# Optimization experiments

Hardware: AMD Instinct MI355X
Metric: run time of the kernel (lower is better)

## Reference

```python
import jax, jax.numpy as jnp
import numpy as np

EMBED_DIM = 768
HEADS = 8
HEAD_DIM = 128  # gnn_hidden_dim
OUT_DIM = HEADS * HEAD_DIM  # 1024, concat=True
NEG_SLOPE = 0.2  # PyG GATConv leaky_relu slope


def setup_inputs() -> dict:
    key = jax.random.key(0)
    ks = jax.random.split(key, 12)
    N, E = 10000, 160000
    x = jax.random.normal(ks[0], (N, EMBED_DIM), dtype=jnp.float32)
    edge_index = jax.random.randint(ks[1], (2, E), 0, N, dtype=jnp.int32)
    edge_attr = jax.random.uniform(ks[2], (E, 1), dtype=jnp.float32)
    # GATConv params (single layer, edge_dim=1)
    sc = 1.0 / np.sqrt(EMBED_DIM)
    W = jax.random.normal(ks[3], (EMBED_DIM, OUT_DIM), dtype=jnp.float32) * sc
    att_src = jax.random.normal(ks[4], (HEADS, HEAD_DIM), dtype=jnp.float32) * 0.1
    att_dst = jax.random.normal(ks[5], (HEADS, HEAD_DIM), dtype=jnp.float32) * 0.1
    W_edge = jax.random.normal(ks[6], (1, OUT_DIM), dtype=jnp.float32)
    att_edge = jax.random.normal(ks[7], (HEADS, HEAD_DIM), dtype=jnp.float32) * 0.1
    bias = jnp.zeros((OUT_DIM,), dtype=jnp.float32)
    # final classifier: in = 3*OUT_DIM (global pool + text node + image node)
    clf_W = jax.random.normal(ks[8], (3 * OUT_DIM, 2), dtype=jnp.float32) * (1.0 / np.sqrt(3 * OUT_DIM))
    clf_b = jnp.zeros((2,), dtype=jnp.float32)
    return {
        'x': x, 'edge_index': edge_index, 'edge_attr': edge_attr,
        'text_idx': 0, 'image_idx': 1,
        'W': W, 'att_src': att_src, 'att_dst': att_dst,
        'W_edge': W_edge, 'att_edge': att_edge, 'bias': bias,
        'clf_W': clf_W, 'clf_b': clf_b,
    }


def gat_layer(x, edge_index, edge_attr, W, att_src, att_dst, W_edge, att_edge, bias):
    N = x.shape[0]
    # add self-loops with edge_attr = mean of existing edge_attr (PyG default fill_value='mean')
    loop = jnp.arange(N, dtype=edge_index.dtype)
    ei = jnp.concatenate([edge_index, jnp.stack([loop, loop])], axis=1)
    ea_mean = jnp.mean(edge_attr, axis=0, keepdims=True)
    ea = jnp.concatenate([edge_attr, jnp.broadcast_to(ea_mean, (N, edge_attr.shape[1]))], axis=0)
    src, dst = ei[0], ei[1]
    xs = (x @ W).reshape(N, HEADS, HEAD_DIM)             # [N, H, C]
    a_src = jnp.einsum('nhc,hc->nh', xs, att_src)        # per-node src logits
    a_dst = jnp.einsum('nhc,hc->nh', xs, att_dst)
    e_emb = (ea @ W_edge).reshape(-1, HEADS, HEAD_DIM)   # [Etot, H, C]
    a_edge = jnp.einsum('ehc,hc->eh', e_emb, att_edge)
    alpha = jax.nn.leaky_relu(a_src[src] + a_dst[dst] + a_edge, NEG_SLOPE)  # [Etot, H]
    # softmax over incoming edges of each dst node
    m = jax.ops.segment_max(alpha, dst, num_segments=N)
    ex = jnp.exp(alpha - m[dst])
    denom = jax.ops.segment_sum(ex, dst, num_segments=N)
    w = ex / denom[dst]                                  # normalized attention [Etot, H]
    msg = xs[src] * w[:, :, None]                        # [Etot, H, C]
    out = jax.ops.segment_sum(msg, dst, num_segments=N)  # [N, H, C]
    return out.reshape(N, OUT_DIM) + bias


def reference(x, edge_index, edge_attr, text_idx, image_idx,
              W, att_src, att_dst, W_edge, att_edge, bias, clf_W, clf_b):
    # single GAT layer (num_gat_layers=1 -> no ELU/dropout after, eval mode)
    h = gat_layer(x, edge_index, edge_attr, W, att_src, att_dst, W_edge, att_edge, bias)
    g = jnp.mean(h, axis=0, keepdims=True)               # global_mean_pool, batch=None
    t = h[text_idx][None, :]
    im = h[image_idx][None, :]
    fused = jnp.concatenate([g, t, im], axis=1)          # [1, 3*OUT_DIM]
    logits = fused @ clf_W + clf_b                       # [1, 2]
    return logits
```

## Files before the change

### kernel.cpp

```cpp
#include <hip/hip_runtime.h>

#define NN 10000
#define EE 160000
#define ETOT (EE + NN)
#define EMB 768
#define ODIM 1024
#define NEG 0.2f
#define CAP 56

#define OFF_P      0
#define OFF_Q      12288
#define OFF_EAP    12296
#define OFF_EAACC  12360
#define OFF_CNTD   12364
#define ZERO_START 12364
#define ZERO_CNT   10000
#define OFF_A      22364
#define OFF_T      182364
#define OFF_SAED   342364
#define OFF_RDEN   1462364
#define OFF_G      1542364

#define SELF_MARK 3.0e38f

__global__ __launch_bounds__(256) void k1a(
    const float* __restrict__ W, const float* __restrict__ att_src,
    const float* __restrict__ att_dst, const float* __restrict__ W_edge,
    const float* __restrict__ att_edge, const float* __restrict__ bias,
    const float* __restrict__ clf_W, const float* __restrict__ clf_b,
    float* __restrict__ out, float* __restrict__ ws) {
  __shared__ float sred[8];
  int b = blockIdx.x;
  if (b < 48) {
    int tid = b * 256 + threadIdx.x;
    int k = tid >> 4, j = tid & 15, h = j & 7;
    const float* att = (j < 8) ? att_src : att_dst;
    const float4* wp = (const float4*)(W + k * ODIM + h * 128);
    const float4* ap = (const float4*)(att + h * 128);
    float acc = 0.f;
    #pragma unroll 8
    for (int c = 0; c < 32; ++c) {
      float4 w4 = wp[c], a4 = ap[c];
      acc += w4.x * a4.x + w4.y * a4.y + w4.z * a4.z + w4.w * a4.w;
    }
    ws[OFF_P + tid] = acc;
  } else if (b == 48) {
    if (threadIdx.x < 8) {
      int h = threadIdx.x;
      float acc = 0.f;
      #pragma unroll 8
      for (int c = 0; c < 128; ++c) acc += W_edge[h * 128 + c] * att_edge[h * 128 + c];
      ws[OFF_Q + h] = acc;
    }
  } else if (b == 49) {
    int t = threadIdx.x;
    float b0 = 0.f, b1 = 0.f;
    for (int i = t; i < 3072; i += 256) {
      float f = bias[i & 1023];
      b0 += f * clf_W[2 * i];
      b1 += f * clf_W[2 * i + 1];
    }
    #pragma unroll
    for (int o = 32; o > 0; o >>= 1) {
      b0 += __shfl_down(b0, o, 64);
      b1 += __shfl_down(b1, o, 64);
    }
    if ((t & 63) == 0) { sred[(t >> 6) * 2] = b0; sred[(t >> 6) * 2 + 1] = b1; }
    __syncthreads();
    if (t == 0) {
      out[0] = clf_b[0] + sred[0] + sred[2] + sred[4] + sred[6];
      out[1] = clf_b[1] + sred[1] + sred[3] + sred[5] + sred[7];
    }
  } else {
    int t = (b - 50) * 256 + threadIdx.x;
    int k = t >> 3, h = t & 7;
    const float4* wseg = (const float4*)(W + k * ODIM + h * 128);
    float acc[6] = {0.f, 0.f, 0.f, 0.f, 0.f, 0.f};
    for (int c4 = 0; c4 < 32; ++c4) {
      float4 wv = wseg[c4];
      #pragma unroll
      for (int d = 0; d < 3; ++d) {
        const float4* cp = (const float4*)(clf_W + 2 * (1024 * d + h * 128 + c4 * 4));
        float4 q0 = cp[0], q1 = cp[1];
        acc[d * 2 + 0] += wv.x * q0.x + wv.y * q0.z + wv.z * q1.x + wv.w * q1.z;
        acc[d * 2 + 1] += wv.x * q0.y + wv.y * q0.w + wv.z * q1.y + wv.w * q1.w;
      }
    }
    #pragma unroll
    for (int d = 0; d < 3; ++d) {
      ws[OFF_G + d * 12288 + k * 16 + h * 2 + 0] = acc[d * 2 + 0];
      ws[OFF_G + d * 12288 + k * 16 + h * 2 + 1] = acc[d * 2 + 1];
    }
  }
}

__global__ __launch_bounds__(256) void k1b(const float* __restrict__ edge_attr,
                                           const int* __restrict__ ei,
                                           float* __restrict__ ws) {
  __shared__ float sred[8];
  int b = blockIdx.x;
  if (b < 64) {
    float acc = 0.f;
    for (int i = b * 256 + threadIdx.x; i < EE; i += 64 * 256) acc += edge_attr[i];
    #pragma unroll
    for (int off = 32; off > 0; off >>= 1) acc += __shfl_down(acc, off, 64);
    if ((threadIdx.x & 63) == 0) sred[threadIdx.x >> 6] = acc;
    __syncthreads();
    if (threadIdx.x == 0)
      ws[OFF_EAP + b] = sred[0] + sred[1] + sred[2] + sred[3];
  } else {
    int e = (b - 64) * 256 + threadIdx.x;
    if (e >= ETOT) return;
    int src, dst; float ea;
    if (e < EE) { src = ei[e]; dst = ei[EE + e]; ea = edge_attr[e]; }
    else { src = dst = e - EE; ea = SELF_MARK; }
    int* cntd = (int*)(ws + OFF_CNTD);
    int pd = atomicAdd(&cntd[dst], 1);
    if (pd < CAP) {
      float2 pr; pr.x = __int_as_float(src); pr.y = ea;
      ((float2*)(ws + OFF_SAED))[dst * CAP + pd] = pr;
    }
  }
}

__global__ __launch_bounds__(256) void kAxT(const float* __restrict__ x,
                                            float* __restrict__ ws) {
  __shared__ float smem[12288];
  if (blockIdx.x == 313) {
    if (threadIdx.x < 64) {
      float v = ws[OFF_EAP + threadIdx.x];
      #pragma unroll
      for (int o = 32; o > 0; o >>= 1) v += __shfl_down(v, o, 64);
      if (threadIdx.x == 0) ws[OFF_EAACC] = v;
    }
    return;
  }
  int nl = threadIdx.x & 31, cg = threadIdx.x >> 5;
  int n = blockIdx.x * 32 + nl;
  #pragma unroll
  for (int pass = 0; pass < 2; ++pass) {
    const int tbl = (pass == 0) ? OFF_P : OFF_G;
    const int dstoff = (pass == 0) ? OFF_A : OFF_T;
    for (int i = threadIdx.x; i < 3072; i += 256)
      ((float4*)smem)[i] = ((const float4*)(ws + tbl))[i];
    __syncthreads();
    float a[16];
    #pragma unroll
    for (int j = 0; j < 16; ++j) a[j] = 0.f;
    if (n < NN) {
      const float4* xr = (const float4*)(x + n * EMB + cg * 96);
      for (int kk = 0; kk < 24; ++kk) {
        float4 xv = xr[kk];
        const float* pr = &smem[(cg * 96 + kk * 4) * 16];
        #pragma unroll
        for (int j = 0; j < 16; ++j) a[j] += xv.x * pr[j];
        #pragma unroll
        for (int j = 0; j < 16; ++j) a[j] += xv.y * pr[16 + j];
        #pragma unroll
        for (int j = 0; j < 16; ++j) a[j] += xv.z * pr[32 + j];
        #pragma unroll
        for (int j = 0; j < 16; ++j) a[j] += xv.w * pr[48 + j];
      }
    }
    __syncthreads();
    #pragma unroll
    for (int j = 0; j < 16; ++j) smem[(cg * 16 + j) * 33 + nl] = a[j];
    __syncthreads();
    for (int w = threadIdx.x; w < 512; w += 256) {
      int rnl = w >> 4, j = w & 15;
      int nn = blockIdx.x * 32 + rnl;
      if (nn < NN) {
        float s = 0.f;
        #pragma unroll
        for (int c2 = 0; c2 < 8; ++c2) s += smem[(c2 * 16 + j) * 33 + rnl];
        ws[dstoff + nn * 16 + j] = s;
      }
    }
    __syncthreads();
  }
}

__global__ __launch_bounds__(128) void kD(float* __restrict__ ws) {
  int t = blockIdx.x * 128 + threadIdx.x;
  int dst = t >> 3, h = t & 7;
  int deg = ((const int*)(ws + OFF_CNTD))[dst];
  if (deg > CAP) deg = CAP;
  float adh = ws[OFF_A + dst * 16 + 8 + h];
  float qh = ws[OFF_Q + h];
  float mean = ws[OFF_EAACC] * (1.0f / EE);
  const float2* prow = (const float2*)(ws + OFF_SAED) + dst * CAP;
  float den = 0.f;
  #pragma unroll 4
  for (int j = 0; j < deg; ++j) {
    float2 pr = prow[j];
    int srcj = __float_as_int(pr.x);
    float ae = pr.y;
    if (ae > 1e37f) ae = mean;
    float v = ws[OFF_A + srcj * 16 + h] + adh + ae * qh;
    v = (v >= 0.f) ? v : NEG * v;
    den += __expf(v);
  }
  ws[OFF_RDEN + t] = 1.0f / den;
}

__global__ __launch_bounds__(256, 3) void kFin(const float* __restrict__ x,
                                               const int* __restrict__ ei,
                                               const float* __restrict__ edge_attr,
                                               const int* __restrict__ tptr,
                                               const int* __restrict__ iptr,
                                               float* __restrict__ out,
                                               float* __restrict__ ws) {
  __shared__ float smem[12864];
  int t = threadIdx.x;
  float mean = ws[OFF_EAACC] * (1.0f / EE);
  float c0 = 0.f, c1 = 0.f;
  float scale;
  if (blockIdx.x < 665) {
    scale = 1.0f / NN;
    int e = blockIdx.x * 256 + t;
    if (e < ETOT) {
      int src, dst; float ea;
      if (e < EE) { src = ei[e]; dst = ei[EE + e]; ea = edge_attr[e]; }
      else { src = dst = e - EE; ea = mean; }
      const float4* as4 = (const float4*)(ws + OFF_A + src * 16);
      const float4* ad4 = (const float4*)(ws + OFF_A + dst * 16 + 8);
      const float4* rd4 = (const float4*)(ws + OFF_RDEN + dst * 8);
      const float4* t4  = (const float4*)(ws + OFF_T + src * 16);
      float4 s0 = as4[0], s1 = as4[1], d0 = ad4[0], d1 = ad4[1];
      float4 r0 = rd4[0], r1 = rd4[1];
      float4 t0 = t4[0], t1 = t4[1], t2 = t4[2], t3 = t4[3];
      float asr[8] = {s0.x, s0.y, s0.z, s0.w, s1.x, s1.y, s1.z, s1.w};
      float ads[8] = {d0.x, d0.y, d0.z, d0.w, d1.x, d1.y, d1.z, d1.w};
      float rdn[8] = {r0.x, r0.y, r0.z, r0.w, r1.x, r1.y, r1.z, r1.w};
      float tt[16] = {t0.x, t0.y, t0.z, t0.w, t1.x, t1.y, t1.z, t1.w,
                      t2.x, t2.y, t2.z, t2.w, t3.x, t3.y, t3.z, t3.w};
      #pragma unroll
      for (int h = 0; h < 8; ++h) {
        float v = asr[h] + ads[h] + ea * ws[OFF_Q + h];
        v = (v >= 0.f) ? v : NEG * v;
        float w = __expf(v) * rdn[h];
        c0 += w * tt[2 * h];
        c1 += w * tt[2 * h + 1];
      }
    }
  } else {
    scale = 1.0f;
    int d = blockIdx.x - 665;
    int target = (d == 0) ? tptr[0] : iptr[0];
    for (int i = t; i < 3072; i += 256)
      ((float4*)smem)[i] = ((const float4*)(ws + OFF_G + (d + 1) * 12288))[i];
    int deg = ((const int*)(ws + OFF_CNTD))[target];
    if (deg > CAP) deg = CAP;
    for (int idx = t; idx < deg * 8; idx += 256) {
      int j = idx >> 3, h = idx & 7;
      float2 pr = ((const float2*)(ws + OFF_SAED))[target * CAP + j];
      int srcj = __float_as_int(pr.x);
      float ae = pr.y;
      if (ae > 1e37f) ae = mean;
      float v = ws[OFF_A + srcj * 16 + h] + ws[OFF_A + target * 16 + 8 + h]
              + ae * ws[OFF_Q + h];
      v = (v >= 0.f) ? v : NEG * v;
      smem[12288 + j * 8 + h] = __expf(v) * ws[OFF_RDEN + target * 8 + h];
      if (h == 0) ((int*)smem)[12800 + j] = srcj;
    }
    __syncthreads();
    int nl = t & 15, cgp = t >> 4;
    for (int jb = 0; jb * 16 < deg; ++jb) {
      int j = jb * 16 + nl;
      int n = (j < deg) ? ((int*)smem)[12800 + j] : 0;
      float a[16];
      #pragma unroll
      for (int jj = 0; jj < 16; ++jj) a[jj] = 0.f;
      const float4* xr = (const float4*)(x + n * EMB + cgp * 48);
      for (int kk = 0; kk < 12; ++kk) {
        float4 xv = xr[kk];
        const float* pr = &smem[(cgp * 48 + kk * 4) * 16];
        #pragma unroll
        for (int jj = 0; jj < 16; ++jj) a[jj] += xv.x * pr[jj];
        #pragma unroll
        for (int jj = 0; jj < 16; ++jj) a[jj] += xv.y * pr[16 + jj];
        #pragma unroll
        for (int jj = 0; jj < 16; ++jj) a[jj] += xv.z * pr[32 + jj];
        #pragma unroll
        for (int jj = 0; jj < 16; ++jj) a[jj] += xv.w * pr[48 + jj];
      }
      if (j < deg) {
        #pragma unroll
        for (int h = 0; h < 8; ++h) {
          float wv = smem[12288 + j * 8 + h];
          c0 += wv * a[2 * h];
          c1 += wv * a[2 * h + 1];
        }
      }
    }
  }
  #pragma unroll
  for (int o = 32; o > 0; o >>= 1) {
    c0 += __shfl_down(c0, o, 64);
    c1 += __shfl_down(c1, o, 64);
  }
  if ((t & 63) == 0) {
    smem[12856 + (t >> 6) * 2] = c0;
    smem[12857 + (t >> 6) * 2] = c1;
  }
  __syncthreads();
  if (t == 0) {
    float r0 = smem[12856] + smem[12858] + smem[12860] + smem[12862];
    float r1 = smem[12857] + smem[12859] + smem[12861] + smem[12863];
    atomicAdd(&out[0], r0 * scale);
    atomicAdd(&out[1], r1 * scale);
  }
}

extern "C" void kernel_launch(void* const* d_in, const int* in_sizes, int n_in,
                              void* d_out, int out_size, void* d_ws, size_t ws_size,
                              hipStream_t stream) {
  const float* x        = (const float*)d_in[0];
  const int*   ei       = (const int*)d_in[1];
  const float* edge_attr= (const float*)d_in[2];
  const int*   tptr     = (const int*)d_in[3];
  const int*   iptr     = (const int*)d_in[4];
  const float* W        = (const float*)d_in[5];
  const float* att_src  = (const float*)d_in[6];
  const float* att_dst  = (const float*)d_in[7];
  const float* W_edge   = (const float*)d_in[8];
  const float* att_edge = (const float*)d_in[9];
  const float* bias     = (const float*)d_in[10];
  const float* clf_W    = (const float*)d_in[11];
  const float* clf_b    = (const float*)d_in[12];
  float* ws  = (float*)d_ws;
  float* out = (float*)d_out;

  hipMemsetAsync(ws + ZERO_START, 0, ZERO_CNT * sizeof(float), stream);
  k1a<<<74, 256, 0, stream>>>(W, att_src, att_dst, W_edge, att_edge,
                              bias, clf_W, clf_b, out, ws);
  k1b<<<729, 256, 0, stream>>>(edge_attr, ei, ws);
  kAxT<<<314, 256, 0, stream>>>(x, ws);
  kD<<<625, 128, 0, stream>>>(ws);
  kFin<<<667, 256, 0, stream>>>(x, ei, edge_attr, tptr, iptr, out, ws);
}
```

Before: 193.2 us.

## Fuse pipeline into three kernels and merge softmax denominator into dst-side aggregation

Replaces the memset and five kernels with three launches. Zeroing of the degree counters moves into k1, and CSR bucketing now runs in the same launch as the x·P/x·G projection (k2). The separate denominator kernel and the per-edge final pass become one per-(dst,head) loop that accumulates the exp sum and the weighted T numerator together, so the reciprocal-denominator buffer and its reread go away. This cuts launch gaps and memory traffic. It risks a race: bucketing in k2 reads counters zeroed in k1, which is fine across launches, but k2's projection and bucketing blocks now share one grid, and the per-dst loop has an uneven per-thread degree load.

```diff
diff --git a/kernel.cpp b/kernel.cpp
--- a/kernel.cpp
+++ b/kernel.cpp
@@ -13,22 +13,20 @@
 #define OFF_EAP    12296
 #define OFF_EAACC  12360
 #define OFF_CNTD   12364
-#define ZERO_START 12364
-#define ZERO_CNT   10000
 #define OFF_A      22364
 #define OFF_T      182364
 #define OFF_SAED   342364
-#define OFF_RDEN   1462364
-#define OFF_G      1542364
+#define OFF_G      1462364
 
 #define SELF_MARK 3.0e38f
 
-__global__ __launch_bounds__(256) void k1a(
+__global__ __launch_bounds__(256) void k1(
     const float* __restrict__ W, const float* __restrict__ att_src,
     const float* __restrict__ att_dst, const float* __restrict__ W_edge,
-    const float* __restrict__ att_edge, const float* __restrict__ bias,
-    const float* __restrict__ clf_W, const float* __restrict__ clf_b,
-    float* __restrict__ out, float* __restrict__ ws) {
+    const float* __restrict__ att_edge, const float* __restrict__ edge_attr,
+    const float* __restrict__ bias, const float* __restrict__ clf_W,
+    const float* __restrict__ clf_b, float* __restrict__ out,
+    float* __restrict__ ws) {
   __shared__ float sred[8];
   int b = blockIdx.x;
   if (b < 48) {
@@ -71,7 +69,7 @@
       out[0] = clf_b[0] + sred[0] + sred[2] + sred[4] + sred[6];
       out[1] = clf_b[1] + sred[1] + sred[3] + sred[5] + sred[7];
     }
-  } else {
+  } else if (b < 74) {
     int t = (b - 50) * 256 + threadIdx.x;
     int k = t >> 3, h = t & 7;
     const float4* wseg = (const float4*)(W + k * ODIM + h * 128);
@@ -91,25 +89,38 @@
       ws[OFF_G + d * 12288 + k * 16 + h * 2 + 0] = acc[d * 2 + 0];
       ws[OFF_G + d * 12288 + k * 16 + h * 2 + 1] = acc[d * 2 + 1];
     }
-  }
-}
-
-__global__ __launch_bounds__(256) void k1b(const float* __restrict__ edge_attr,
-                                           const int* __restrict__ ei,
-                                           float* __restrict__ ws) {
-  __shared__ float sred[8];
-  int b = blockIdx.x;
-  if (b < 64) {
+  } else if (b < 138) {
+    int bi = b - 74;
     float acc = 0.f;
-    for (int i = b * 256 + threadIdx.x; i < EE; i += 64 * 256) acc += edge_attr[i];
+    for (int i = bi * 256 + threadIdx.x; i < EE; i += 64 * 256) acc += edge_attr[i];
     #pragma unroll
     for (int off = 32; off > 0; off >>= 1) acc += __shfl_down(acc, off, 64);
     if ((threadIdx.x & 63) == 0) sred[threadIdx.x >> 6] = acc;
     __syncthreads();
     if (threadIdx.x == 0)
-      ws[OFF_EAP + b] = sred[0] + sred[1] + sred[2] + sred[3];
+      ws[OFF_EAP + bi] = sred[0] + sred[1] + sred[2] + sred[3];
   } else {
-    int e = (b - 64) * 256 + threadIdx.x;
+    int i = (b - 138) * 256 + threadIdx.x;
+    if (i < NN) ((int*)(ws + OFF_CNTD))[i] = 0;
+  }
+}
+
+__global__ __launch_bounds__(256) void k2(const float* __restrict__ x,
+                                          const int* __restrict__ ei,
+                                          const float* __restrict__ edge_attr,
+                                          float* __restrict__ ws) {
+  __shared__ float smem[12288];
+  if (blockIdx.x == 313) {
+    if (threadIdx.x < 64) {
+      float v = ws[OFF_EAP + threadIdx.x];
+      #pragma unroll
+      for (int o = 32; o > 0; o >>= 1) v += __shfl_down(v, o, 64);
+      if (threadIdx.x == 0) ws[OFF_EAACC] = v;
+    }
+    return;
+  }
+  if (blockIdx.x >= 314) {
+    int e = (blockIdx.x - 314) * 256 + threadIdx.x;
     if (e >= ETOT) return;
     int src, dst; float ea;
     if (e < EE) { src = ei[e]; dst = ei[EE + e]; ea = edge_attr[e]; }
@@ -120,19 +131,6 @@
       float2 pr; pr.x = __int_as_float(src); pr.y = ea;
       ((float2*)(ws + OFF_SAED))[dst * CAP + pd] = pr;
     }
-  }
-}
-
-__global__ __launch_bounds__(256) void kAxT(const float* __restrict__ x,
-                                            float* __restrict__ ws) {
-  __shared__ float smem[12288];
-  if (blockIdx.x == 313) {
-    if (threadIdx.x < 64) {
-      float v = ws[OFF_EAP + threadIdx.x];
-      #pragma unroll
-      for (int o = 32; o > 0; o >>= 1) v += __shfl_down(v, o, 64);
-      if (threadIdx.x == 0) ws[OFF_EAACC] = v;
-    }
     return;
   }
   int nl = threadIdx.x & 31, cg = threadIdx.x >> 5;
@@ -180,72 +178,48 @@
   }
 }
 
-__global__ __launch_bounds__(128) void kD(float* __restrict__ ws) {
-  int t = blockIdx.x * 128 + threadIdx.x;
-  int dst = t >> 3, h = t & 7;
-  int deg = ((const int*)(ws + OFF_CNTD))[dst];
-  if (deg > CAP) deg = CAP;
-  float adh = ws[OFF_A + dst * 16 + 8 + h];
-  float qh = ws[OFF_Q + h];
-  float mean = ws[OFF_EAACC] * (1.0f / EE);
-  const float2* prow = (const float2*)(ws + OFF_SAED) + dst * CAP;
-  float den = 0.f;
-  #pragma unroll 4
-  for (int j = 0; j < deg; ++j) {
-    float2 pr = prow[j];
-    int srcj = __float_as_int(pr.x);
-    float ae = pr.y;
-    if (ae > 1e37f) ae = mean;
-    float v = ws[OFF_A + srcj * 16 + h] + adh + ae * qh;
-    v = (v >= 0.f) ? v : NEG * v;
-    den += __expf(v);
-  }
-  ws[OFF_RDEN + t] = 1.0f / den;
-}
-
-__global__ __launch_bounds__(256, 3) void kFin(const float* __restrict__ x,
-                                               const int* __restrict__ ei,
-                                               const float* __restrict__ edge_attr,
-                                               const int* __restrict__ tptr,
-                                               const int* __restrict__ iptr,
-                                               float* __restrict__ out,
-                                               float* __restrict__ ws) {
-  __shared__ float smem[12864];
+__global__ __launch_bounds__(256, 3) void k3(const float* __restrict__ x,
+                                             const int* __restrict__ tptr,
+                                             const int* __restrict__ iptr,
+                                             float* __restrict__ out,
+                                             float* __restrict__ ws) {
+  __shared__ float smem[12880];
   int t = threadIdx.x;
   float mean = ws[OFF_EAACC] * (1.0f / EE);
   float c0 = 0.f, c1 = 0.f;
   float scale;
-  if (blockIdx.x < 665) {
+  if (blockIdx.x < 313) {
     scale = 1.0f / NN;
-    int e = blockIdx.x * 256 + t;
-    if (e < ETOT) {
-      int src, dst; float ea;
-      if (e < EE) { src = ei[e]; dst = ei[EE + e]; ea = edge_attr[e]; }
-      else { src = dst = e - EE; ea = mean; }
-      const float4* as4 = (const float4*)(ws + OFF_A + src * 16);
-      const float4* ad4 = (const float4*)(ws + OFF_A + dst * 16 + 8);
-      const float4* rd4 = (const float4*)(ws + OFF_RDEN + dst * 8);
-      const float4* t4  = (const float4*)(ws + OFF_T + src * 16);
-      float4 s0 = as4[0], s1 = as4[1], d0 = ad4[0], d1 = ad4[1];
-      float4 r0 = rd4[0], r1 = rd4[1];
-      float4 t0 = t4[0], t1 = t4[1], t2 = t4[2], t3 = t4[3];
-      float asr[8] = {s0.x, s0.y, s0.z, s0.w, s1.x, s1.y, s1.z, s1.w};
-      float ads[8] = {d0.x, d0.y, d0.z, d0.w, d1.x, d1.y, d1.z, d1.w};
-      float rdn[8] = {r0.x, r0.y, r0.z, r0.w, r1.x, r1.y, r1.z, r1.w};
-      float tt[16] = {t0.x, t0.y, t0.z, t0.w, t1.x, t1.y, t1.z, t1.w,
-                      t2.x, t2.y, t2.z, t2.w, t3.x, t3.y, t3.z, t3.w};
-      #pragma unroll
-      for (int h = 0; h < 8; ++h) {
-        float v = asr[h] + ads[h] + ea * ws[OFF_Q + h];
+    int tk = blockIdx.x * 256 + t;
+    if (tk < 80000) {
+      int dst = tk >> 3, h = tk & 7;
+      int deg = ((const int*)(ws + OFF_CNTD))[dst];
+      if (deg > CAP) deg = CAP;
+      float adh = ws[OFF_A + dst * 16 + 8 + h];
+      float qh = ws[OFF_Q + h];
+      const float2* prow = (const float2*)(ws + OFF_SAED) + dst * CAP;
+      float den = 0.f, n0 = 0.f, n1 = 0.f;
+      #pragma unroll 4
+      for (int j = 0; j < deg; ++j) {
+        float2 pr = prow[j];
+        int srcj = __float_as_int(pr.x);
+        float ae = pr.y;
+        if (ae > 1e37f) ae = mean;
+        float v = ws[OFF_A + srcj * 16 + h] + adh + ae * qh;
         v = (v >= 0.f) ? v : NEG * v;
-        float w = __expf(v) * rdn[h];
-        c0 += w * tt[2 * h];
-        c1 += w * tt[2 * h + 1];
-      }
+        float ex = __expf(v);
+        den += ex;
+        float2 tv = *(const float2*)(ws + OFF_T + srcj * 16 + 2 * h);
+        n0 += ex * tv.x;
+        n1 += ex * tv.y;
+      }
+      float r = 1.0f / den;
+      c0 = n0 * r;
+      c1 = n1 * r;
     }
   } else {
     scale = 1.0f;
-    int d = blockIdx.x - 665;
+    int d = blockIdx.x - 313;
     int target = (d == 0) ? tptr[0] : iptr[0];
     for (int i = t; i < 3072; i += 256)
       ((float4*)smem)[i] = ((const float4*)(ws + OFF_G + (d + 1) * 12288))[i];
@@ -260,8 +234,14 @@
       float v = ws[OFF_A + srcj * 16 + h] + ws[OFF_A + target * 16 + 8 + h]
               + ae * ws[OFF_Q + h];
       v = (v >= 0.f) ? v : NEG * v;
-      smem[12288 + j * 8 + h] = __expf(v) * ws[OFF_RDEN + target * 8 + h];
+      smem[12288 + j * 8 + h] = __expf(v);
       if (h == 0) ((int*)smem)[12800 + j] = srcj;
+    }
+    __syncthreads();
+    if (t < 8) {
+      float den = 0.f;
+      for (int j = 0; j < deg; ++j) den += smem[12288 + j * 8 + t];
+      smem[12872 + t] = 1.0f / den;
     }
     __syncthreads();
     int nl = t & 15, cgp = t >> 4;
@@ -287,7 +267,7 @@
       if (j < deg) {
         #pragma unroll
         for (int h = 0; h < 8; ++h) {
-          float wv = smem[12288 + j * 8 + h];
+          float wv = smem[12288 + j * 8 + h] * smem[12872 + h];
           c0 += wv * a[2 * h];
           c1 += wv * a[2 * h + 1];
         }
@@ -331,11 +311,8 @@
   float* ws  = (float*)d_ws;
   float* out = (float*)d_out;
 
-  hipMemsetAsync(ws + ZERO_START, 0, ZERO_CNT * sizeof(float), stream);
-  k1a<<<74, 256, 0, stream>>>(W, att_src, att_dst, W_edge, att_edge,
+  k1<<<178, 256, 0, stream>>>(W, att_src, att_dst, W_edge, att_edge, edge_attr,
                               bias, clf_W, clf_b, out, ws);
-  k1b<<<729, 256, 0, stream>>>(edge_attr, ei, ws);
-  kAxT<<<314, 256, 0, stream>>>(x, ws);
-  kD<<<625, 128, 0, stream>>>(ws);
-  kFin<<<667, 256, 0, stream>>>(x, ei, edge_attr, tptr, iptr, out, ws);
+  k2<<<979, 256, 0, stream>>>(x, ei, edge_attr, ws);
+  k3<<<315, 256, 0, stream>>>(x, tptr, iptr, out, ws);
 }
```

Result: faster. 167.3 us (-13.4%).
